# Kernel tuning notes

Measured on AMD Instinct MI355X. Metric: run time of the kernel, lower is better.

Reference implementation:

```python
import jax, jax.numpy as jnp
import numpy as np

# Fixed Gauss-Legendre quadrature on [-A, A] replacing scipy.integrate.quadrature
A = 5.0
NQ = 64
_x, _w = np.polynomial.legendre.leggauss(NQ)
GL_X = jnp.asarray(_x * A, dtype=jnp.float32)  # nodes scaled to [-5, 5]
# Fold exp(-z^2/2)/sqrt(2*pi) and interval scaling into the weights
GL_W_EFF = jnp.asarray(_w * A * np.exp(-(_x * A) ** 2 / 2.0) / np.sqrt(2.0 * np.pi), dtype=jnp.float32)

# given_params=True constants
SIG_M1, SIG_M2, SIG_I = 1.0, 1.0, 1.0
SIG_M1N1, SIG_M2N2 = 1.0, 0.5
SIG_N1I, SIG_N2I = 0.5, 1.9
SIG_M1W, SIG_M2W = 2.8, -2.2
TAU, DT = 100.0, 20.0


def setup_inputs() -> dict:
    key = jax.random.key(0)
    B, T = 8192, 2048
    u = jax.random.normal(key, (B, T), dtype=jnp.float32)
    return {"u": u}


def reference(u):
    B, T = u.shape
    alpha = jnp.float32(DT / TAU)

    def step(carry, u_t):
        k1, k2, v = carry  # each [B]
        delta = jnp.sqrt(SIG_M1**2 * k1**2 + SIG_M2**2 * k2**2 + SIG_I**2 * u_t**2)  # [B]
        # gauss_int[b] = int_{-A}^{A} (1 - tanh(delta_b z)^2) exp(-z^2/2) dz / sqrt(2pi)
        dphi = 1.0 - jnp.tanh(delta[:, None] * GL_X[None, :]) ** 2  # [B, NQ]
        gauss_int = dphi @ GL_W_EFF  # [B]
        k1_new = k1 + (-k1 + SIG_M1N1 * gauss_int * k1 + SIG_N1I * gauss_int * v) * alpha
        k2_new = k2 + (-k2 + SIG_M2N2 * gauss_int * k2 + SIG_N2I * gauss_int * v) * alpha
        v_new = v + (-v + u_t) * alpha
        z = SIG_M1W * k1_new + SIG_M2W * k2_new
        return (k1_new, k2_new, v_new), z

    zeros = jnp.zeros((B,), dtype=u.dtype)
    _, z_seq = jax.lax.scan(step, (zeros, zeros, zeros), u.T)  # z_seq: [T, B]
    # z_hist: [B, T+1], column 0 is the zero initial state
    z_hist = jnp.concatenate([zeros[:, None], z_seq.T], axis=1)
    return z_hist
```

## Files before the change

kernel.cpp:

```cpp
#include <hip/hip_runtime.h>
#include <math.h>


#define Bsz   8192
#define Tlen  2048
#define TP1   2049
#define NQ    64
#define NG    2049
#define NTAB2 2048
#define INV_H 32.0f
#define CHUNKS 16
#define CLEN  128
#define WARM  128
#define BLOCK 256
#define SIM_GRID (32 * CHUNKS)

#define WS_TAB 128

__device__ __forceinline__ void bar_nodrain() {
    asm volatile("s_waitcnt lgkmcnt(0)" ::: "memory");
    __builtin_amdgcn_s_barrier();
}

__global__ __launch_bounds__(256) void setup_kernel(float* __restrict__ ws,
                                                    float* __restrict__ out) {
    __shared__ float  fx[NQ], fw[NQ];
    __shared__ double inv[NQ + 1];
    const int tid = threadIdx.x;
    if (tid <= NQ) inv[tid] = (tid == 0) ? 0.0 : 1.0 / (double)tid;
    __syncthreads();
    if (tid < NQ) {
        double z = cos(3.14159265358979323846 * (tid + 0.75) / (NQ + 0.5));
        double p1 = 1.0, p2 = 0.0, pp = 1.0;
        for (int it = 0; it < 4; ++it) {
            p1 = 1.0; p2 = 0.0;
            for (int j = 1; j <= NQ; ++j) {
                double p3 = p2; p2 = p1;
                p1 = ((2.0 * j - 1.0) * z * p2 - (j - 1.0) * p3) * inv[j];
            }
            pp = NQ * (z * p1 - p2) / (z * z - 1.0);
            if (it < 3) z -= p1 / pp;
        }
        double w  = 2.0 / ((1.0 - z * z) * pp * pp);
        double xs = z * 5.0;
        fx[tid] = (float)xs;
        fw[tid] = (float)(w * 5.0 * exp(-0.5 * xs * xs) * 0.3989422804014327);
    }
    __syncthreads();
    const int j = blockIdx.x * BLOCK + tid;
    if (j < NG) {
        const float d = sqrtf((float)j * (1.0f / INV_H));
        float acc = 0.0f;
        #pragma unroll 8
        for (int q = 0; q < NQ; ++q) {
            float t = tanhf(d * fx[q]);
            acc = fmaf(fw[q], 1.0f - t * t, acc);
        }
        ws[WS_TAB + j] = acc;
    }
    out[(size_t)j * TP1] = 0.0f;
}

__device__ __forceinline__ float step_one(float uu, float& k1, float& k2,
                                          float& v, const float2* s_tab) {
    float s   = fmaf(k1, k1, fmaf(k2, k2, uu * uu));
    float idx = fminf(s * INV_H, 2046.999f);
    int   i0  = (int)idx;
    float f   = idx - (float)i0;
    float2 g2 = s_tab[i0];
    float g   = fmaf(f, g2.y - g2.x, g2.x);
    float gv  = g * v;
    float nk1 = fmaf(k1, fmaf(0.2f, g, 0.8f), 0.10f * gv);
    float nk2 = fmaf(k2, fmaf(0.1f, g, 0.8f), 0.38f * gv);
    v  = fmaf(0.2f, uu - v, v);
    k1 = nk1; k2 = nk2;
    return fmaf(2.8f, nk1, -2.2f * nk2);
}

__global__ __launch_bounds__(BLOCK, 2) void sim_kernel(const float* __restrict__ u,
                                                       const float* __restrict__ ws,
                                                       float* __restrict__ out) {
    __shared__ float2 s_tab[NTAB2];
    __shared__ __align__(16) float s_ovl[64 * 65];
    float2 (*s_u2)[BLOCK] = (float2 (*)[BLOCK])s_ovl;
    float* s_zt = s_ovl;
    const int tid = threadIdx.x;

    const int c    = blockIdx.x >> 5;
    const int bb   = blockIdx.x & 31;
    const int rowb = bb * BLOCK;
    const int t_out   = c * CLEN;
    const int t_begin = (t_out >= WARM) ? (t_out - WARM) : 0;

    const int r1 = tid >> 1;
    const int h4 = (tid & 1) * 4;
    const int ph = (tid & 1) * 2;
    const float* __restrict__ upb = u + (size_t)(rowb + r1) * Tlen + h4;

    float4 Ua0 = *(const float4*)(upb + t_begin);
    float4 Ub0 = *(const float4*)(upb + t_begin + 128 * Tlen);
    float4 Ua1 = *(const float4*)(upb + t_begin + 8);
    float4 Ub1 = *(const float4*)(upb + t_begin + 8 + 128 * Tlen);

    {
        const float* g = ws + WS_TAB;
        #pragma unroll
        for (int i = 0; i < NTAB2 / (BLOCK * 4); ++i) {
            int k = (i * BLOCK + tid) * 4;
            float4 a = *(const float4*)(g + k);
            float  b = g[k + 4];
            s_tab[k + 0] = make_float2(a.x, a.y);
            s_tab[k + 1] = make_float2(a.y, a.z);
            s_tab[k + 2] = make_float2(a.z, a.w);
            s_tab[k + 3] = make_float2(a.w, b);
        }
    }

    float k1 = 0.f, k2 = 0.f, v = 0.f;

    for (int tb = t_begin; tb < t_out; tb += 8) {
        bar_nodrain();
        s_u2[ph    ][r1      ] = make_float2(Ua0.x, Ua0.y);
        s_u2[ph + 1][r1      ] = make_float2(Ua0.z, Ua0.w);
        s_u2[ph    ][r1 + 128] = make_float2(Ub0.x, Ub0.y);
        s_u2[ph + 1][r1 + 128] = make_float2(Ub0.z, Ub0.w);
        Ua0 = Ua1; Ub0 = Ub1;
        const int tn = tb + 16;
        Ua1 = *(const float4*)(upb + tn);
        Ub1 = *(const float4*)(upb + tn + 128 * Tlen);
        bar_nodrain();
        #pragma unroll
        for (int p = 0; p < 4; ++p) {
            float2 uu = s_u2[p][tid];
            step_one(uu.x, k1, k2, v, s_tab);
            step_one(uu.y, k1, k2, v, s_tab);
        }
    }

    const int myw = tid >> 6;
    const int lr  = tid & 63;
    for (int h = 0; h < 2; ++h) {
        float zz[64];
        #pragma unroll
        for (int gq = 0; gq < 8; ++gq) {
            const int tb = t_out + h * 64 + gq * 8;
            bar_nodrain();
            s_u2[ph    ][r1      ] = make_float2(Ua0.x, Ua0.y);
            s_u2[ph + 1][r1      ] = make_float2(Ua0.z, Ua0.w);
            s_u2[ph    ][r1 + 128] = make_float2(Ub0.x, Ub0.y);
            s_u2[ph + 1][r1 + 128] = make_float2(Ub0.z, Ub0.w);
            Ua0 = Ua1; Ub0 = Ub1;
            int tn = tb + 16;
            if (tn > Tlen - 8) tn = Tlen - 8;
            Ua1 = *(const float4*)(upb + tn);
            Ub1 = *(const float4*)(upb + tn + 128 * Tlen);
            bar_nodrain();
            #pragma unroll
            for (int p = 0; p < 4; ++p) {
                float2 uu = s_u2[p][tid];
                zz[gq * 8 + 2 * p    ] = step_one(uu.x, k1, k2, v, s_tab);
                zz[gq * 8 + 2 * p + 1] = step_one(uu.y, k1, k2, v, s_tab);
            }
        }
        const int cb = t_out + 1 + h * 64;
        for (int p4 = 0; p4 < 4; ++p4) {
            bar_nodrain();
            if (myw == p4) {
                #pragma unroll
                for (int j = 0; j < 64; ++j)
                    s_zt[lr * 65 + j] = zz[j];
            }
            bar_nodrain();
            #pragma unroll
            for (int k = 0; k < 16; ++k) {
                int d   = tid + 256 * k;
                int row = d >> 6;
                int col = d & 63;
                out[(size_t)(rowb + p4 * 64 + row) * TP1 + cb + col] =
                    s_zt[row * 65 + col];
            }
        }
    }
}

extern "C" void kernel_launch(void* const* d_in, const int* in_sizes, int n_in,
                              void* d_out, int out_size, void* d_ws, size_t ws_size,
                              hipStream_t stream) {
    const float* u = (const float*)d_in[0];
    float* out = (float*)d_out;
    float* ws  = (float*)d_ws;
    setup_kernel<<<32, BLOCK, 0, stream>>>(ws, out);
    sim_kernel<<<SIM_GRID, BLOCK, 0, stream>>>(u, ws, out);
}
```

Measured before the change: 150.0 us.

## Process two independent rows per thread to interleave serial recurrences

Each thread now advances two independent batch rows (A and B) in lockstep, so the dependent table-lookup and FMA chains of one row can hide the latency of the other. Blocks cover 512 rows, which halves the grid to 256 blocks, and the launch bound drops to one block per SM. The output transpose is redone in 32-column tiles with a padded 33-stride LDS buffer. The cost is higher register pressure and fewer blocks and waves to hide memory latency, with 256 blocks on a 256-CU part.

After: 163.4 us. +8.9%, slower.

```diff
diff --git a/kernel.cpp b/kernel.cpp
--- a/kernel.cpp
+++ b/kernel.cpp
@@ -13,7 +13,9 @@
 #define CLEN  128
 #define WARM  128
 #define BLOCK 256
-#define SIM_GRID (32 * CHUNKS)
+#define ROWS_PB 512
+#define NRB   16
+#define SIM_GRID (NRB * CHUNKS)
 
 #define WS_TAB 128
 
@@ -47,7 +49,7 @@
         fw[tid] = (float)(w * 5.0 * exp(-0.5 * xs * xs) * 0.3989422804014327);
     }
     __syncthreads();
-    const int j = blockIdx.x * BLOCK + tid;
+    const int j = blockIdx.x * 256 + tid;
     if (j < NG) {
         const float d = sqrtf((float)j * (1.0f / INV_H));
         float acc = 0.0f;
@@ -61,34 +63,49 @@
     out[(size_t)j * TP1] = 0.0f;
 }
 
-__device__ __forceinline__ float step_one(float uu, float& k1, float& k2,
-                                          float& v, const float2* s_tab) {
-    float s   = fmaf(k1, k1, fmaf(k2, k2, uu * uu));
-    float idx = fminf(s * INV_H, 2046.999f);
-    int   i0  = (int)idx;
-    float f   = idx - (float)i0;
-    float2 g2 = s_tab[i0];
-    float g   = fmaf(f, g2.y - g2.x, g2.x);
-    float gv  = g * v;
-    float nk1 = fmaf(k1, fmaf(0.2f, g, 0.8f), 0.10f * gv);
-    float nk2 = fmaf(k2, fmaf(0.1f, g, 0.8f), 0.38f * gv);
-    v  = fmaf(0.2f, uu - v, v);
-    k1 = nk1; k2 = nk2;
-    return fmaf(2.8f, nk1, -2.2f * nk2);
-}
-
-__global__ __launch_bounds__(BLOCK, 2) void sim_kernel(const float* __restrict__ u,
+__device__ __forceinline__ void step_pair(float uA, float uB,
+                                          float& k1A, float& k2A, float& vA,
+                                          float& k1B, float& k2B, float& vB,
+                                          const float2* s_tab,
+                                          float& zA, float& zB) {
+    float sA   = fmaf(k1A, k1A, fmaf(k2A, k2A, uA * uA));
+    float sB   = fmaf(k1B, k1B, fmaf(k2B, k2B, uB * uB));
+    float idxA = fminf(sA * INV_H, 2046.999f);
+    float idxB = fminf(sB * INV_H, 2046.999f);
+    int   i0A  = (int)idxA;
+    int   i0B  = (int)idxB;
+    float2 gA  = s_tab[i0A];
+    float2 gB  = s_tab[i0B];
+    float fA   = idxA - (float)i0A;
+    float fB   = idxB - (float)i0B;
+    float gxA  = fmaf(fA, gA.y - gA.x, gA.x);
+    float gxB  = fmaf(fB, gB.y - gB.x, gB.x);
+    float gvA  = gxA * vA;
+    float gvB  = gxB * vB;
+    float nk1A = fmaf(k1A, fmaf(0.2f, gxA, 0.8f), 0.10f * gvA);
+    float nk1B = fmaf(k1B, fmaf(0.2f, gxB, 0.8f), 0.10f * gvB);
+    float nk2A = fmaf(k2A, fmaf(0.1f, gxA, 0.8f), 0.38f * gvA);
+    float nk2B = fmaf(k2B, fmaf(0.1f, gxB, 0.8f), 0.38f * gvB);
+    vA = fmaf(0.2f, uA - vA, vA);
+    vB = fmaf(0.2f, uB - vB, vB);
+    k1A = nk1A; k2A = nk2A;
+    k1B = nk1B; k2B = nk2B;
+    zA = fmaf(2.8f, nk1A, -2.2f * nk2A);
+    zB = fmaf(2.8f, nk1B, -2.2f * nk2B);
+}
+
+__global__ __launch_bounds__(BLOCK, 1) void sim_kernel(const float* __restrict__ u,
                                                        const float* __restrict__ ws,
                                                        float* __restrict__ out) {
     __shared__ float2 s_tab[NTAB2];
-    __shared__ __align__(16) float s_ovl[64 * 65];
-    float2 (*s_u2)[BLOCK] = (float2 (*)[BLOCK])s_ovl;
-    float* s_zt = s_ovl;
+    __shared__ __align__(16) char s_ovl[256 * 33 * 4];
+    float2 (*s_u2)[ROWS_PB] = (float2 (*)[ROWS_PB])s_ovl;
+    float* s_zt = (float*)s_ovl;
     const int tid = threadIdx.x;
 
-    const int c    = blockIdx.x >> 5;
-    const int bb   = blockIdx.x & 31;
-    const int rowb = bb * BLOCK;
+    const int c    = blockIdx.x >> 4;
+    const int bb   = blockIdx.x & 15;
+    const int rowb = bb * ROWS_PB;
     const int t_out   = c * CLEN;
     const int t_begin = (t_out >= WARM) ? (t_out - WARM) : 0;
 
@@ -96,11 +113,16 @@
     const int h4 = (tid & 1) * 4;
     const int ph = (tid & 1) * 2;
     const float* __restrict__ upb = u + (size_t)(rowb + r1) * Tlen + h4;
-
-    float4 Ua0 = *(const float4*)(upb + t_begin);
-    float4 Ub0 = *(const float4*)(upb + t_begin + 128 * Tlen);
-    float4 Ua1 = *(const float4*)(upb + t_begin + 8);
-    float4 Ub1 = *(const float4*)(upb + t_begin + 8 + 128 * Tlen);
+    const int RO = 128 * Tlen;
+
+    float4 A0 = *(const float4*)(upb + t_begin);
+    float4 A1 = *(const float4*)(upb + t_begin + RO);
+    float4 A2 = *(const float4*)(upb + t_begin + 2 * RO);
+    float4 A3 = *(const float4*)(upb + t_begin + 3 * RO);
+    float4 B0 = *(const float4*)(upb + t_begin + 8);
+    float4 B1 = *(const float4*)(upb + t_begin + 8 + RO);
+    float4 B2 = *(const float4*)(upb + t_begin + 8 + 2 * RO);
+    float4 B3 = *(const float4*)(upb + t_begin + 8 + 3 * RO);
 
     {
         const float* g = ws + WS_TAB;
@@ -116,69 +138,90 @@
         }
     }
 
-    float k1 = 0.f, k2 = 0.f, v = 0.f;
+    float k1A = 0.f, k2A = 0.f, vA = 0.f;
+    float k1B = 0.f, k2B = 0.f, vB = 0.f;
 
     for (int tb = t_begin; tb < t_out; tb += 8) {
         bar_nodrain();
-        s_u2[ph    ][r1      ] = make_float2(Ua0.x, Ua0.y);
-        s_u2[ph + 1][r1      ] = make_float2(Ua0.z, Ua0.w);
-        s_u2[ph    ][r1 + 128] = make_float2(Ub0.x, Ub0.y);
-        s_u2[ph + 1][r1 + 128] = make_float2(Ub0.z, Ub0.w);
-        Ua0 = Ua1; Ub0 = Ub1;
+        s_u2[ph    ][r1      ] = make_float2(A0.x, A0.y);
+        s_u2[ph + 1][r1      ] = make_float2(A0.z, A0.w);
+        s_u2[ph    ][r1 + 128] = make_float2(A1.x, A1.y);
+        s_u2[ph + 1][r1 + 128] = make_float2(A1.z, A1.w);
+        s_u2[ph    ][r1 + 256] = make_float2(A2.x, A2.y);
+        s_u2[ph + 1][r1 + 256] = make_float2(A2.z, A2.w);
+        s_u2[ph    ][r1 + 384] = make_float2(A3.x, A3.y);
+        s_u2[ph + 1][r1 + 384] = make_float2(A3.z, A3.w);
+        A0 = B0; A1 = B1; A2 = B2; A3 = B3;
         const int tn = tb + 16;
-        Ua1 = *(const float4*)(upb + tn);
-        Ub1 = *(const float4*)(upb + tn + 128 * Tlen);
-        bar_nodrain();
+        B0 = *(const float4*)(upb + tn);
+        B1 = *(const float4*)(upb + tn + RO);
+        B2 = *(const float4*)(upb + tn + 2 * RO);
+        B3 = *(const float4*)(upb + tn + 3 * RO);
+        bar_nodrain();
+        float zs0, zs1;
         #pragma unroll
         for (int p = 0; p < 4; ++p) {
-            float2 uu = s_u2[p][tid];
-            step_one(uu.x, k1, k2, v, s_tab);
-            step_one(uu.y, k1, k2, v, s_tab);
-        }
-    }
-
-    const int myw = tid >> 6;
-    const int lr  = tid & 63;
-    for (int h = 0; h < 2; ++h) {
-        float zz[64];
-        #pragma unroll
-        for (int gq = 0; gq < 8; ++gq) {
-            const int tb = t_out + h * 64 + gq * 8;
+            float2 ua = s_u2[p][tid];
+            float2 ub = s_u2[p][tid + 256];
+            step_pair(ua.x, ub.x, k1A, k2A, vA, k1B, k2B, vB, s_tab, zs0, zs1);
+            step_pair(ua.y, ub.y, k1A, k2A, vA, k1B, k2B, vB, s_tab, zs0, zs1);
+        }
+    }
+
+    const int col = tid & 31;
+    const int rq  = tid >> 5;
+    for (int q = 0; q < 4; ++q) {
+        float zz_a[32], zz_b[32];
+        #pragma unroll
+        for (int it4 = 0; it4 < 4; ++it4) {
+            const int tb = t_out + q * 32 + it4 * 8;
             bar_nodrain();
-            s_u2[ph    ][r1      ] = make_float2(Ua0.x, Ua0.y);
-            s_u2[ph + 1][r1      ] = make_float2(Ua0.z, Ua0.w);
-            s_u2[ph    ][r1 + 128] = make_float2(Ub0.x, Ub0.y);
-            s_u2[ph + 1][r1 + 128] = make_float2(Ub0.z, Ub0.w);
-            Ua0 = Ua1; Ub0 = Ub1;
+            s_u2[ph    ][r1      ] = make_float2(A0.x, A0.y);
+            s_u2[ph + 1][r1      ] = make_float2(A0.z, A0.w);
+            s_u2[ph    ][r1 + 128] = make_float2(A1.x, A1.y);
+            s_u2[ph + 1][r1 + 128] = make_float2(A1.z, A1.w);
+            s_u2[ph    ][r1 + 256] = make_float2(A2.x, A2.y);
+            s_u2[ph + 1][r1 + 256] = make_float2(A2.z, A2.w);
+            s_u2[ph    ][r1 + 384] = make_float2(A3.x, A3.y);
+            s_u2[ph + 1][r1 + 384] = make_float2(A3.z, A3.w);
+            A0 = B0; A1 = B1; A2 = B2; A3 = B3;
             int tn = tb + 16;
             if (tn > Tlen - 8) tn = Tlen - 8;
-            Ua1 = *(const float4*)(upb + tn);
-            Ub1 = *(const float4*)(upb + tn + 128 * Tlen);
+            B0 = *(const float4*)(upb + tn);
+            B1 = *(const float4*)(upb + tn + RO);
+            B2 = *(const float4*)(upb + tn + 2 * RO);
+            B3 = *(const float4*)(upb + tn + 3 * RO);
             bar_nodrain();
             #pragma unroll
             for (int p = 0; p < 4; ++p) {
-                float2 uu = s_u2[p][tid];
-                zz[gq * 8 + 2 * p    ] = step_one(uu.x, k1, k2, v, s_tab);
-                zz[gq * 8 + 2 * p + 1] = step_one(uu.y, k1, k2, v, s_tab);
+                float2 ua = s_u2[p][tid];
+                float2 ub = s_u2[p][tid + 256];
+                step_pair(ua.x, ub.x, k1A, k2A, vA, k1B, k2B, vB, s_tab,
+                          zz_a[it4 * 8 + 2 * p    ], zz_b[it4 * 8 + 2 * p    ]);
+                step_pair(ua.y, ub.y, k1A, k2A, vA, k1B, k2B, vB, s_tab,
+                          zz_a[it4 * 8 + 2 * p + 1], zz_b[it4 * 8 + 2 * p + 1]);
             }
         }
-        const int cb = t_out + 1 + h * 64;
-        for (int p4 = 0; p4 < 4; ++p4) {
-            bar_nodrain();
-            if (myw == p4) {
-                #pragma unroll
-                for (int j = 0; j < 64; ++j)
-                    s_zt[lr * 65 + j] = zz[j];
-            }
-            bar_nodrain();
-            #pragma unroll
-            for (int k = 0; k < 16; ++k) {
-                int d   = tid + 256 * k;
-                int row = d >> 6;
-                int col = d & 63;
-                out[(size_t)(rowb + p4 * 64 + row) * TP1 + cb + col] =
-                    s_zt[row * 65 + col];
-            }
+        const int cb = t_out + 1 + q * 32;
+        bar_nodrain();
+        #pragma unroll
+        for (int j = 0; j < 32; ++j)
+            s_zt[tid * 33 + j] = zz_a[j];
+        bar_nodrain();
+        #pragma unroll
+        for (int k = 0; k < 32; ++k) {
+            int row = k * 8 + rq;
+            out[(size_t)(rowb + row) * TP1 + cb + col] = s_zt[row * 33 + col];
+        }
+        bar_nodrain();
+        #pragma unroll
+        for (int j = 0; j < 32; ++j)
+            s_zt[tid * 33 + j] = zz_b[j];
+        bar_nodrain();
+        #pragma unroll
+        for (int k = 0; k < 32; ++k) {
+            int row = k * 8 + rq;
+            out[(size_t)(rowb + 256 + row) * TP1 + cb + col] = s_zt[row * 33 + col];
         }
     }
 }
@@ -189,6 +232,6 @@
     const float* u = (const float*)d_in[0];
     float* out = (float*)d_out;
     float* ws  = (float*)d_ws;
-    setup_kernel<<<32, BLOCK, 0, stream>>>(ws, out);
+    setup_kernel<<<32, 256, 0, stream>>>(ws, out);
     sim_kernel<<<SIM_GRID, BLOCK, 0, stream>>>(u, ws, out);
 }
```

## Stage input per-wavefront in 32-step tiles to drop block-wide barriers

Applied to the files above, without the earlier changes.

Each wavefront now owns a private LDS staging tile for its 64 rows. It loads 32 timesteps per row with wide float4 loads into registers and double-buffers them, so the per-8-step block barriers are replaced by wave-local lgkmcnt waits. The output transpose is also done per wavefront, with no block barriers. The intent is to cut barrier stalls and load issue overhead, at the cost of much higher register use (two 8-entry float4 buffers plus zz[64]), which may hurt occupancy or spill, and it relies on intra-wave LDS ordering being correct without barriers.

After: 145.0 us. 1.03x faster.

```diff
diff --git a/kernel.cpp b/kernel.cpp
--- a/kernel.cpp
+++ b/kernel.cpp
@@ -14,12 +14,16 @@
 #define WARM  128
 #define BLOCK 256
 #define SIM_GRID (32 * CHUNKS)
+#define SROW  33
 
 #define WS_TAB 128
 
 __device__ __forceinline__ void bar_nodrain() {
     asm volatile("s_waitcnt lgkmcnt(0)" ::: "memory");
     __builtin_amdgcn_s_barrier();
+}
+__device__ __forceinline__ void ds_fence() {
+    asm volatile("s_waitcnt lgkmcnt(0)" ::: "memory");
 }
 
 __global__ __launch_bounds__(256) void setup_kernel(float* __restrict__ ws,
@@ -47,7 +51,7 @@
         fw[tid] = (float)(w * 5.0 * exp(-0.5 * xs * xs) * 0.3989422804014327);
     }
     __syncthreads();
-    const int j = blockIdx.x * BLOCK + tid;
+    const int j = blockIdx.x * 256 + tid;
     if (j < NG) {
         const float d = sqrtf((float)j * (1.0f / INV_H));
         float acc = 0.0f;
@@ -77,30 +81,41 @@
     return fmaf(2.8f, nk1, -2.2f * nk2);
 }
 
+#define GLOAD(G, t) { _Pragma("unroll")                                       \
+    for (int r = 0; r < 8; ++r)                                               \
+        G[r] = *(const float4*)(up + (size_t)r * 8 * Tlen + (t)); }
+
+#define STAGE(G) { asm volatile("" ::: "memory");  _Pragma("unroll")          \
+    for (int r = 0; r < 8; ++r) {                                             \
+        int b8 = (8 * r + srow) * SROW + scol;                                \
+        sb[b8] = G[r].x; sb[b8+1] = G[r].y; sb[b8+2] = G[r].z;                \
+        sb[b8+3] = G[r].w; }                                                  \
+    ds_fence(); }
+
 __global__ __launch_bounds__(BLOCK, 2) void sim_kernel(const float* __restrict__ u,
                                                        const float* __restrict__ ws,
                                                        float* __restrict__ out) {
     __shared__ float2 s_tab[NTAB2];
-    __shared__ __align__(16) float s_ovl[64 * 65];
-    float2 (*s_u2)[BLOCK] = (float2 (*)[BLOCK])s_ovl;
-    float* s_zt = s_ovl;
+    __shared__ float  s_st[4][64 * SROW];
     const int tid = threadIdx.x;
+    const int w   = tid >> 6;
+    const int l   = tid & 63;
+    float* sb = s_st[w];
 
     const int c    = blockIdx.x >> 5;
     const int bb   = blockIdx.x & 31;
-    const int rowb = bb * BLOCK;
+    const int rowb = bb * 256 + w * 64;
     const int t_out   = c * CLEN;
     const int t_begin = (t_out >= WARM) ? (t_out - WARM) : 0;
 
-    const int r1 = tid >> 1;
-    const int h4 = (tid & 1) * 4;
-    const int ph = (tid & 1) * 2;
-    const float* __restrict__ upb = u + (size_t)(rowb + r1) * Tlen + h4;
+    const int srow = l >> 3;
+    const int scol = (l & 7) * 4;
+    const float* __restrict__ up = u + (size_t)(rowb + srow) * Tlen + scol;
+    const int lbase = l * SROW;
 
-    float4 Ua0 = *(const float4*)(upb + t_begin);
-    float4 Ub0 = *(const float4*)(upb + t_begin + 128 * Tlen);
-    float4 Ua1 = *(const float4*)(upb + t_begin + 8);
-    float4 Ub1 = *(const float4*)(upb + t_begin + 8 + 128 * Tlen);
+    float4 G0[8], G1[8];
+    GLOAD(G0, t_begin);
+    GLOAD(G1, t_begin + 32);
 
     {
         const float* g = ws + WS_TAB;
@@ -115,70 +130,59 @@
             s_tab[k + 3] = make_float2(a.w, b);
         }
     }
+    bar_nodrain();
 
     float k1 = 0.f, k2 = 0.f, v = 0.f;
 
-    for (int tb = t_begin; tb < t_out; tb += 8) {
-        bar_nodrain();
-        s_u2[ph    ][r1      ] = make_float2(Ua0.x, Ua0.y);
-        s_u2[ph + 1][r1      ] = make_float2(Ua0.z, Ua0.w);
-        s_u2[ph    ][r1 + 128] = make_float2(Ub0.x, Ub0.y);
-        s_u2[ph + 1][r1 + 128] = make_float2(Ub0.z, Ub0.w);
-        Ua0 = Ua1; Ub0 = Ub1;
-        const int tn = tb + 16;
-        Ua1 = *(const float4*)(upb + tn);
-        Ub1 = *(const float4*)(upb + tn + 128 * Tlen);
-        bar_nodrain();
+    for (int tb = t_begin; tb + 64 <= t_out; tb += 64) {
+        STAGE(G0);
+        GLOAD(G0, tb + 64);
         #pragma unroll
-        for (int p = 0; p < 4; ++p) {
-            float2 uu = s_u2[p][tid];
-            step_one(uu.x, k1, k2, v, s_tab);
-            step_one(uu.y, k1, k2, v, s_tab);
-        }
+        for (int t2 = 0; t2 < 32; ++t2)
+            step_one(sb[lbase + t2], k1, k2, v, s_tab);
+        STAGE(G1);
+        GLOAD(G1, tb + 96);
+        #pragma unroll
+        for (int t2 = 0; t2 < 32; ++t2)
+            step_one(sb[lbase + t2], k1, k2, v, s_tab);
     }
 
-    const int myw = tid >> 6;
-    const int lr  = tid & 63;
+    const int col = l & 31;
+    const int rh  = l >> 5;
     for (int h = 0; h < 2; ++h) {
         float zz[64];
-        #pragma unroll
-        for (int gq = 0; gq < 8; ++gq) {
-            const int tb = t_out + h * 64 + gq * 8;
-            bar_nodrain();
-            s_u2[ph    ][r1      ] = make_float2(Ua0.x, Ua0.y);
-            s_u2[ph + 1][r1      ] = make_float2(Ua0.z, Ua0.w);
-            s_u2[ph    ][r1 + 128] = make_float2(Ub0.x, Ub0.y);
-            s_u2[ph + 1][r1 + 128] = make_float2(Ub0.z, Ub0.w);
-            Ua0 = Ua1; Ub0 = Ub1;
-            int tn = tb + 16;
-            if (tn > Tlen - 8) tn = Tlen - 8;
-            Ua1 = *(const float4*)(upb + tn);
-            Ub1 = *(const float4*)(upb + tn + 128 * Tlen);
-            bar_nodrain();
+        const int tb = t_out + h * 64;
+        {
+            STAGE(G0);
+            int tn = tb + 64; if (tn > Tlen - 32) tn = Tlen - 32;
+            GLOAD(G0, tn);
             #pragma unroll
-            for (int p = 0; p < 4; ++p) {
-                float2 uu = s_u2[p][tid];
-                zz[gq * 8 + 2 * p    ] = step_one(uu.x, k1, k2, v, s_tab);
-                zz[gq * 8 + 2 * p + 1] = step_one(uu.y, k1, k2, v, s_tab);
-            }
+            for (int t2 = 0; t2 < 32; ++t2)
+                zz[t2] = step_one(sb[lbase + t2], k1, k2, v, s_tab);
+        }
+        {
+            STAGE(G1);
+            int tn = tb + 96; if (tn > Tlen - 32) tn = Tlen - 32;
+            GLOAD(G1, tn);
+            #pragma unroll
+            for (int t2 = 0; t2 < 32; ++t2)
+                zz[32 + t2] = step_one(sb[lbase + t2], k1, k2, v, s_tab);
         }
         const int cb = t_out + 1 + h * 64;
-        for (int p4 = 0; p4 < 4; ++p4) {
-            bar_nodrain();
-            if (myw == p4) {
-                #pragma unroll
-                for (int j = 0; j < 64; ++j)
-                    s_zt[lr * 65 + j] = zz[j];
+        #pragma unroll
+        for (int p = 0; p < 2; ++p) {
+            asm volatile("" ::: "memory");
+            #pragma unroll
+            for (int j = 0; j < 32; ++j)
+                sb[lbase + j] = zz[p * 32 + j];
+            ds_fence();
+            #pragma unroll
+            for (int k = 0; k < 32; ++k) {
+                int row = 2 * k + rh;
+                out[(size_t)(rowb + row) * TP1 + cb + p * 32 + col] =
+                    sb[row * SROW + col];
             }
-            bar_nodrain();
-            #pragma unroll
-            for (int k = 0; k < 16; ++k) {
-                int d   = tid + 256 * k;
-                int row = d >> 6;
-                int col = d & 63;
-                out[(size_t)(rowb + p4 * 64 + row) * TP1 + cb + col] =
-                    s_zt[row * 65 + col];
-            }
+            ds_fence();
         }
     }
 }
@@ -189,6 +193,6 @@
     const float* u = (const float*)d_in[0];
     float* out = (float*)d_out;
     float* ws  = (float*)d_ws;
-    setup_kernel<<<32, BLOCK, 0, stream>>>(ws, out);
+    setup_kernel<<<32, 256, 0, stream>>>(ws, out);
     sim_kernel<<<SIM_GRID, BLOCK, 0, stream>>>(u, ws, out);
 }
```
